# Optimization experiments

Measured on AMD Instinct MI355X. Metric: run time of the kernel, lower is better.

## Reference

```python
import jax, jax.numpy as jnp
import numpy as np

N = 20000      # nodes
E = 320000     # edges (avg degree 16)
DIN, H1, H2, DOUT = 256, 256, 128, 64


def _lin_params(key, din, dout):
    kw, kb = jax.random.split(key)
    s = 1.0 / np.sqrt(din)
    W = jax.random.uniform(kw, (din, dout), jnp.float32, -s, s)
    b = jax.random.uniform(kb, (dout,), jnp.float32, -s, s)
    return W, b


def setup_inputs() -> dict:
    key = jax.random.key(0)
    keys = jax.random.split(key, 20)
    inp = {
        'x': jax.random.normal(keys[0], (N, DIN), jnp.float32),
        'edge_index': jax.random.randint(keys[1], (2, E), 0, N, jnp.int64),
    }
    dims = [(DIN, H1), (DIN, H1), (DIN, H1),   # layer1 key/query/value
            (H1, H2), (H1, H2), (H1, H2),      # layer2
            (H2, DOUT), (H2, DOUT), (H2, DOUT)]  # layer3
    names = ['k1', 'q1', 'v1', 'k2', 'q2', 'v2', 'k3', 'q3', 'v3']
    for i, (nm, (di, do)) in enumerate(zip(names, dims)):
        W, b = _lin_params(keys[2 + i], di, do)
        inp[nm + '_w'] = W
        inp[nm + '_b'] = b
    # skip (root) weights, no bias per PyG, plus per-conv output bias
    for j, (di, do) in enumerate([(DIN, H1), (H1, H2), (H2, DOUT)], start=1):
        s = 1.0 / np.sqrt(di)
        inp[f's{j}_w'] = jax.random.uniform(keys[11 + 2 * j], (di, do), jnp.float32, -s, s)
        inp[f'bias{j}'] = jnp.zeros((do,), jnp.float32)
    return inp


def _res_gated_conv(x, src, dst, kw, kb, qw, qb, vw, vb, sw, bias):
    # PyG ResGatedGraphConv (flow source_to_target, aggr='add', act=Sigmoid):
    # out_i = lin_skip(x_i) + sum_{j->i} sigmoid(lin_key(x_i) + lin_query(x_j)) * lin_value(x_j) + bias
    k = x @ kw + kb            # [N, D]
    q = x @ qw + qb
    v = x @ vw + vb
    eta = jax.nn.sigmoid(k[dst] + q[src])   # [E, D] edge gate
    msg = eta * v[src]                      # [E, D]
    agg = jax.ops.segment_sum(msg, dst, num_segments=N)  # scatter-add to targets
    return x @ sw + agg + bias


def reference(x, edge_index,
              k1_w, k1_b, q1_w, q1_b, v1_w, v1_b,
              k2_w, k2_b, q2_w, q2_b, v2_w, v2_b,
              k3_w, k3_b, q3_w, q3_b, v3_w, v3_b,
              s1_w, bias1, s2_w, bias2, s3_w, bias3):
    src, dst = edge_index[0], edge_index[1]
    h = _res_gated_conv(x, src, dst, k1_w, k1_b, q1_w, q1_b, v1_w, v1_b, s1_w, bias1)
    # dropout (eval mode -> identity)
    h = _res_gated_conv(h, src, dst, k2_w, k2_b, q2_w, q2_b, v2_w, v2_b, s2_w, bias2)
    h = _res_gated_conv(h, src, dst, k3_w, k3_b, q3_w, q3_b, v3_w, v3_b, s3_w, bias3)
    return jax.nn.softmax(h, axis=1)
```

## Files before the change

### kernel.cpp

```cpp
#include <hip/hip_runtime.h>
#include <hip/hip_bf16.h>
#include <type_traits>


#define NN 20000
#define EE 320000
#define ELLW 64

typedef _Float16 half8 __attribute__((ext_vector_type(8)));
typedef _Float16 half4 __attribute__((ext_vector_type(4)));
typedef _Float16 half2v __attribute__((ext_vector_type(2)));
typedef float f32x4 __attribute__((ext_vector_type(4)));

__device__ __forceinline__ _Float16 f2h(float f) { return (_Float16)f; }
__device__ __forceinline__ float fsigmoid_mul(float v, float x) {
    return v * __builtin_amdgcn_rcpf(1.f + __expf(-x));
}

struct PrepArgs {
    const float* w[3][4];
    const float* b[3][4];
    _Float16* wt[3];
    float* cb[3];
};

__global__ __launch_bounds__(256) void setup_all_kernel(
    const int* __restrict__ ei, int* __restrict__ deg, int* __restrict__ flag,
    const float* __restrict__ x, _Float16* __restrict__ Xh, PrepArgs a) {
    const int b = blockIdx.x;
    const int tid = threadIdx.x;
    if (b < 79) {
        const int i = b * 256 + tid;
        if (i < NN) deg[i] = 0;
    } else if (b == 79) {
        __shared__ int nz;
        if (tid == 0) nz = 0;
        __syncthreads();
        int c = 0;
        for (int t = tid; t < 1024; t += 256)
            if (ei[2 * t + 1] != 0) c = 1;
        if (c) atomicAdd(&nz, 1);
        __syncthreads();
        if (tid == 0) *flag = (nz == 0) ? 1 : 0;
    } else if (b < 1744) {
        const int idx = (b - 80) * 256 + tid;
        int layer, li, K, D, s;
        if (idx < 262144) {
            layer = 0; li = idx; K = 256; D = 256; s = 2;
        } else if (idx < 393216) {
            layer = 1; li = idx - 262144; K = 256; D = 128; s = 1;
        } else {
            layer = 2; li = idx - 393216; K = 128; D = 64; s = 0;
        }
        const int p = li / K;
        const int k = li - p * K;
        const int DV = D >> 6;
        int grp, c;
        if (p < D) {
            grp = 0; c = p;
        } else if (p < 3 * D) {
            const int t = p - D;
            const int g = t >> (s + 1);
            const int r = t & (2 * DV - 1);
            if (r < DV) { grp = 1; c = g * DV + r; }
            else        { grp = 2; c = g * DV + r - DV; }
        } else {
            grp = 3; c = p - 3 * D;
        }
        a.wt[layer][(size_t)p * K + k] =
            f2h(a.w[layer][grp][(size_t)k * D + c]);
        if (k == 0) a.cb[layer][p] = a.b[layer][grp][c];
    } else {
        const int i = ((b - 1744) * 256 + tid) * 8;
        if (i < NN * 256) {
            const float4 f0 = *(const float4*)(x + i);
            const float4 f1 = *(const float4*)(x + i + 4);
            half8 h;
            h[0] = f2h(f0.x); h[1] = f2h(f0.y); h[2] = f2h(f0.z); h[3] = f2h(f0.w);
            h[4] = f2h(f1.x); h[5] = f2h(f1.y); h[6] = f2h(f1.z); h[7] = f2h(f1.w);
            *(half8*)(Xh + i) = h;
        }
    }
}

__device__ __forceinline__ void gemm_tile(
    int bm, int bn, const _Float16* __restrict__ A,
    const _Float16* __restrict__ Bt, const float* __restrict__ catbias,
    _Float16* __restrict__ O, int M, int K, int N) {
    __shared__ _Float16 As[2][4096];
    __shared__ _Float16 Bs[2][4096];

    const int tid = threadIdx.x;
    const int wid = tid >> 6;
    const int lane = tid & 63;
    const int tile_m = bm * 128;
    const int tile_n = bn * 128;
    const int wm = (wid & 1) * 64;
    const int wn = (wid >> 1) * 64;

    const int st_row = (wid << 4) + (lane >> 2);
    const int st_kc = (lane & 3) << 3;

    auto stage = [&](int buf, int kt) {
#pragma unroll
        for (int j = 0; j < 2; ++j) {
            int ar = tile_m + j * 64 + st_row;
            ar = ar < M ? ar : M - 1;
            const _Float16* ag = A + (size_t)ar * K + kt + st_kc;
            __builtin_amdgcn_global_load_lds(
                (const __attribute__((address_space(1))) unsigned int*)ag,
                (__attribute__((address_space(3))) unsigned int*)
                    &As[buf][j * 2048 + (wid << 9)],
                16, 0, 0);
            const int br = tile_n + j * 64 + st_row;
            const _Float16* bg = Bt + (size_t)br * K + kt + st_kc;
            __builtin_amdgcn_global_load_lds(
                (const __attribute__((address_space(1))) unsigned int*)bg,
                (__attribute__((address_space(3))) unsigned int*)
                    &Bs[buf][j * 2048 + (wid << 9)],
                16, 0, 0);
        }
    };

    stage(0, 0);

    f32x4 acc[4][4] = {};
    const int fr = lane & 15;
    const int fk = (lane >> 4) << 3;
    const int niter = K >> 5;

    for (int it = 0; it < niter; ++it) {
        __syncthreads();
        if (it + 1 < niter) stage((it + 1) & 1, (it + 1) << 5);
        const _Float16* as = As[it & 1];
        const _Float16* bs = Bs[it & 1];
        half8 af[4], bf[4];
#pragma unroll
        for (int mi = 0; mi < 4; ++mi)
            af[mi] = *(const half8*)&as[(wm + mi * 16 + fr) * 32 + fk];
#pragma unroll
        for (int ni = 0; ni < 4; ++ni)
            bf[ni] = *(const half8*)&bs[(wn + ni * 16 + fr) * 32 + fk];
#pragma unroll
        for (int mi = 0; mi < 4; ++mi)
#pragma unroll
            for (int ni = 0; ni < 4; ++ni)
                acc[mi][ni] = __builtin_amdgcn_mfma_f32_16x16x32_f16(
                    af[mi], bf[ni], acc[mi][ni], 0, 0, 0);
    }
    __syncthreads();

    _Float16* zone = &As[0][0] + wid * 2048;
    const int cl = lane & 15;
    const int rq = (lane >> 4) << 2;
    const int col0 = tile_n + wn;
    const int r0 = tile_m + wm;
#pragma unroll
    for (int mi = 0; mi < 4; ++mi) {
#pragma unroll
        for (int ni = 0; ni < 4; ++ni) {
            const float cb = catbias[col0 + ni * 16 + cl];
#pragma unroll
            for (int r = 0; r < 4; ++r)
                zone[(rq + r) * 72 + ni * 16 + cl] = f2h(acc[mi][ni][r] + cb);
        }
#pragma unroll
        for (int j = 0; j < 2; ++j) {
            const int rr = j * 8 + (lane >> 3);
            const int row = r0 + mi * 16 + rr;
            const half8 v = *(const half8*)&zone[rr * 72 + (lane & 7) * 8];
            if (row < M)
                *(half8*)&O[(size_t)row * N + col0 + (lane & 7) * 8] = v;
        }
    }
}

__global__ __launch_bounds__(256) void gemm_kernel(
    const _Float16* __restrict__ A, const _Float16* __restrict__ Bt,
    const float* __restrict__ catbias, _Float16* __restrict__ O, int M, int K,
    int N, int mblocks) {
    gemm_tile(blockIdx.x % mblocks, blockIdx.x / mblocks, A, Bt, catbias, O, M,
              K, N);
}

__global__ __launch_bounds__(256) void gemm1_fill_kernel(
    const _Float16* __restrict__ A, const _Float16* __restrict__ Bt,
    const float* __restrict__ catbias, _Float16* __restrict__ O,
    const int* __restrict__ ei, const int* __restrict__ i64flag,
    int* __restrict__ deg, int* __restrict__ col) {
    if (blockIdx.x < 1256) {
        gemm_tile(blockIdx.x % 157, blockIdx.x / 157, A, Bt, catbias, O, NN,
                  256, 1024);
        return;
    }
    const int e = (blockIdx.x - 1256) * 256 + threadIdx.x;
    if (e >= EE) return;
    int src, dst;
    if (*i64flag) {
        const long long* p = (const long long*)ei;
        src = (int)p[e];
        dst = (int)p[EE + e];
    } else {
        src = ei[e];
        dst = ei[EE + e];
    }
    const int pos = atomicAdd(&deg[dst], 1);
    if (pos < ELLW) col[dst * ELLW + pos] = src;
}

template <int D, int MODE>
__global__ __launch_bounds__(256) void edge_gather_kernel(
    const int* __restrict__ deg, const int* __restrict__ col,
    const _Float16* __restrict__ KQVS, _Float16* __restrict__ Hh,
    float* __restrict__ out, int n) {
    constexpr int DV = D / 64;
    constexpr int D4 = 4 * D;
    using qv_t = typename std::conditional<
        DV == 4, half8,
        typename std::conditional<DV == 2, half4, half2v>::type>::type;

    const int node = blockIdx.x * 4 + (threadIdx.x >> 6);
    if (node >= n) return;
    const int lane = threadIdx.x & 63;
    const int ld = lane * DV;

    int dg = deg[node];
    dg = dg < ELLW ? dg : ELLW;
    int idx = col[node * ELLW + lane];
    if (lane >= dg) idx = node;

    float k[DV], acc[DV];
    {
        const _Float16* kp = KQVS + (size_t)node * D4 + ld;
        if constexpr (DV == 4) {
            const half4 u = *(const half4*)kp;
#pragma unroll
            for (int j = 0; j < 4; ++j) k[j] = (float)u[j];
        } else if constexpr (DV == 2) {
            const half2v u = *(const half2v*)kp;
            k[0] = (float)u[0]; k[1] = (float)u[1];
        } else {
            k[0] = (float)*kp;
        }
    }
#pragma unroll
    for (int j = 0; j < DV; ++j) acc[j] = 0.f;

    const _Float16* qvbase = KQVS + D + 2 * ld;
    auto qvacc = [&](qv_t u) {
#pragma unroll
        for (int j = 0; j < DV; ++j)
            acc[j] += fsigmoid_mul((float)u[DV + j], k[j] + (float)u[j]);
    };

    for (int e = 0; e < dg; e += 8) {
        qv_t u[8];
#pragma unroll
        for (int j = 0; j < 8; ++j) {
            const int s = __shfl(idx, e + j, 64);
            u[j] = *(const qv_t*)(qvbase + (size_t)s * D4);
        }
        const int nb = dg - e;
#pragma unroll
        for (int j = 0; j < 8; ++j)
            if (j < nb) qvacc(u[j]);
    }

    float h[DV];
    {
        const _Float16* sp = KQVS + (size_t)node * D4 + 3 * D + ld;
        if constexpr (DV == 4) {
            const half4 u = *(const half4*)sp;
#pragma unroll
            for (int j = 0; j < 4; ++j) h[j] = (float)u[j] + acc[j];
        } else if constexpr (DV == 2) {
            const half2v u = *(const half2v*)sp;
            h[0] = (float)u[0] + acc[0];
            h[1] = (float)u[1] + acc[1];
        } else {
            h[0] = (float)*sp + acc[0];
        }
    }

    if constexpr (MODE == 0) {
        _Float16* op = Hh + (size_t)node * D + ld;
        if constexpr (DV == 4) {
            half4 o;
#pragma unroll
            for (int j = 0; j < 4; ++j) o[j] = f2h(h[j]);
            *(half4*)op = o;
        } else if constexpr (DV == 2) {
            half2v o;
            o[0] = f2h(h[0]); o[1] = f2h(h[1]);
            *(half2v*)op = o;
        } else {
            op[0] = f2h(h[0]);
        }
    } else {
        static_assert(MODE == 0 || DV == 1, "softmax fusion needs D==64");
        float m = h[0];
#pragma unroll
        for (int off = 32; off > 0; off >>= 1)
            m = fmaxf(m, __shfl_xor(m, off, 64));
        const float ex = __expf(h[0] - m);
        float sm = ex;
#pragma unroll
        for (int off = 32; off > 0; off >>= 1) sm += __shfl_xor(sm, off, 64);
        out[(size_t)node * 64 + lane] = ex * __builtin_amdgcn_rcpf(sm);
    }
}

extern "C" void kernel_launch(void* const* d_in, const int* in_sizes, int n_in,
                              void* d_out, int out_size, void* d_ws,
                              size_t ws_size, hipStream_t stream) {
    const float* x = (const float*)d_in[0];
    const int* ei = (const int*)d_in[1];

    char* w = (char*)d_ws;
    _Float16* Xh = (_Float16*)w;     w += (size_t)NN * 256 * 2;
    _Float16* KQVS = (_Float16*)w;   w += (size_t)NN * 1024 * 2;
    _Float16* H1h = (_Float16*)w;    w += (size_t)NN * 256 * 2;
    _Float16* H2h = (_Float16*)w;    w += (size_t)NN * 128 * 2;
    _Float16* Wt1 = (_Float16*)w;    w += (size_t)1024 * 256 * 2;
    _Float16* Wt2 = (_Float16*)w;    w += (size_t)512 * 256 * 2;
    _Float16* Wt3 = (_Float16*)w;    w += (size_t)256 * 128 * 2;
    float* cb1 = (float*)w;          w += 1024 * 4;
    float* cb2 = (float*)w;          w += 512 * 4;
    float* cb3 = (float*)w;          w += 256 * 4;
    int* i64flag = (int*)w;          w += 16;
    int* deg = (int*)w;              w += (size_t)NN * 4;
    int* ell = (int*)w;              w += (size_t)NN * ELLW * 4;

    const dim3 blk(256);
    const int gblocks = (NN + 3) / 4;

    PrepArgs pa;
    pa.w[0][0] = (const float*)d_in[2];  pa.b[0][0] = (const float*)d_in[3];
    pa.w[0][1] = (const float*)d_in[4];  pa.b[0][1] = (const float*)d_in[5];
    pa.w[0][2] = (const float*)d_in[6];  pa.b[0][2] = (const float*)d_in[7];
    pa.w[1][0] = (const float*)d_in[8];  pa.b[1][0] = (const float*)d_in[9];
    pa.w[1][1] = (const float*)d_in[10]; pa.b[1][1] = (const float*)d_in[11];
    pa.w[1][2] = (const float*)d_in[12]; pa.b[1][2] = (const float*)d_in[13];
    pa.w[2][0] = (const float*)d_in[14]; pa.b[2][0] = (const float*)d_in[15];
    pa.w[2][1] = (const float*)d_in[16]; pa.b[2][1] = (const float*)d_in[17];
    pa.w[2][2] = (const float*)d_in[18]; pa.b[2][2] = (const float*)d_in[19];
    pa.w[0][3] = (const float*)d_in[20]; pa.b[0][3] = (const float*)d_in[21];
    pa.w[1][3] = (const float*)d_in[22]; pa.b[1][3] = (const float*)d_in[23];
    pa.w[2][3] = (const float*)d_in[24]; pa.b[2][3] = (const float*)d_in[25];
    pa.wt[0] = Wt1; pa.wt[1] = Wt2; pa.wt[2] = Wt3;
    pa.cb[0] = cb1; pa.cb[1] = cb2; pa.cb[2] = cb3;

    setup_all_kernel<<<4244, blk, 0, stream>>>(ei, deg, i64flag, x, Xh, pa);

    gemm1_fill_kernel<<<2506, blk, 0, stream>>>(Xh, Wt1, cb1, KQVS, ei,
                                                i64flag, deg, ell);
    edge_gather_kernel<256, 0><<<gblocks, blk, 0, stream>>>(
        deg, ell, KQVS, H1h, nullptr, NN);

    gemm_kernel<<<157 * 4, blk, 0, stream>>>(H1h, Wt2, cb2, KQVS, NN, 256, 512,
                                             157);
    edge_gather_kernel<128, 0><<<gblocks, blk, 0, stream>>>(
        deg, ell, KQVS, H2h, nullptr, NN);

    gemm_kernel<<<157 * 2, blk, 0, stream>>>(H2h, Wt3, cb3, KQVS, NN, 128, 256,
                                             157);
    edge_gather_kernel<64, 1><<<gblocks, blk, 0, stream>>>(
        deg, ell, KQVS, nullptr, (float*)d_out, NN);
}
```

Before: 259.5 us.

## Double-buffer neighbor gathers in edge_gather_kernel with readlane indices

Restructures the per-node edge loop into a ping-pong software pipeline. The next batch of 8 neighbor q/v loads is issued before the current batch's sigmoid-gated accumulation, with scheduling barriers so the compiler keeps that order. The neighbor index is now broadcast with readlane instead of a shuffle, and the launch bounds request 4 blocks per CU. The goal is to hide gather latency behind compute, at the cost of twice the registers for loaded data, which the occupancy hint may restrict.

```diff
diff --git a/kernel.cpp b/kernel.cpp
--- a/kernel.cpp
+++ b/kernel.cpp
@@ -209,7 +209,7 @@
 }
 
 template <int D, int MODE>
-__global__ __launch_bounds__(256) void edge_gather_kernel(
+__global__ __launch_bounds__(256, 4) void edge_gather_kernel(
     const int* __restrict__ deg, const int* __restrict__ col,
     const _Float16* __restrict__ KQVS, _Float16* __restrict__ Hh,
     float* __restrict__ out, int n) {
@@ -246,24 +246,56 @@
 #pragma unroll
     for (int j = 0; j < DV; ++j) acc[j] = 0.f;
 
-    const _Float16* qvbase = KQVS + D + 2 * ld;
-    auto qvacc = [&](qv_t u) {
+    auto ldqv = [&](qv_t& u, int e) {
+        const int s = __builtin_amdgcn_readlane(idx, e);
+        const qv_t* p = (const qv_t*)(KQVS + (size_t)s * D4 + D) + lane;
+        u = *p;
+    };
+    auto edgeacc = [&](qv_t u) {
 #pragma unroll
         for (int j = 0; j < DV; ++j)
             acc[j] += fsigmoid_mul((float)u[DV + j], k[j] + (float)u[j]);
     };
 
-    for (int e = 0; e < dg; e += 8) {
-        qv_t u[8];
-#pragma unroll
-        for (int j = 0; j < 8; ++j) {
-            const int s = __shfl(idx, e + j, 64);
-            u[j] = *(const qv_t*)(qvbase + (size_t)s * D4);
-        }
-        const int nb = dg - e;
+    qv_t ua[8], ub[8];
+    auto issue = [&](qv_t* u, int e0) {
+#pragma unroll
+        for (int j = 0; j < 8; ++j) ldqv(u[j], e0 + j);
+    };
+    auto consume8 = [&](qv_t* u) {
+#pragma unroll
+        for (int j = 0; j < 8; ++j) edgeacc(u[j]);
+    };
+    auto consume_tail = [&](qv_t* u, int nb) {
 #pragma unroll
         for (int j = 0; j < 8; ++j)
-            if (j < nb) qvacc(u[j]);
+            if (j < nb) edgeacc(u[j]);
+    };
+
+    if (dg > 0) {
+        issue(ua, 0);
+        for (int e = 0;;) {
+            int nb = dg - e;
+            if (nb <= 8) {
+                __builtin_amdgcn_sched_barrier(0);
+                consume_tail(ua, nb);
+                break;
+            }
+            issue(ub, e + 8);
+            __builtin_amdgcn_sched_barrier(0);
+            consume8(ua);
+            e += 8;
+            nb = dg - e;
+            if (nb <= 8) {
+                __builtin_amdgcn_sched_barrier(0);
+                consume_tail(ub, nb);
+                break;
+            }
+            issue(ua, e + 8);
+            __builtin_amdgcn_sched_barrier(0);
+            consume8(ub);
+            e += 8;
+        }
     }
 
     float h[DV];
```

After: 256.7 us, median of 2. No clear change (-1.1%).
